# Optimization experiments

Hardware: AMD Instinct MI355X
Metric: run time of the kernel (lower is better)

## Reference

```python
import jax, jax.numpy as jnp
import numpy as np

S, D, H, E = 4096, 1024, 16, 64  # seq_len, embed_dim, n_heads, head_size


def setup_inputs() -> dict:
    key = jax.random.key(0)
    ks = jax.random.split(key, 8)
    s_d = 1.0 / np.sqrt(D).astype(np.float32)
    return {
        "x": jax.random.normal(ks[0], (S, D), jnp.float32),
        # per-head Q/K/V projections (no bias), stacked over heads: [H, D, E]
        "Wk": jax.random.normal(ks[1], (H, D, E), jnp.float32) * s_d,
        "Wq": jax.random.normal(ks[2], (H, D, E), jnp.float32) * s_d,
        "Wv": jax.random.normal(ks[3], (H, D, E), jnp.float32) * s_d,
        # output projection Dense(D) with bias
        "Wo": jax.random.normal(ks[4], (H * E, D), jnp.float32) * (1.0 / np.sqrt(H * E).astype(np.float32)),
        "bo": jnp.zeros((D,), jnp.float32),
        # MLP: Dense(4D) -> gelu -> Dense(D), both with bias
        "W1": jax.random.normal(ks[5], (D, 4 * D), jnp.float32) * s_d,
        "b1": jnp.zeros((4 * D,), jnp.float32),
        "W2": jax.random.normal(ks[6], (4 * D, D), jnp.float32) * (1.0 / np.sqrt(4 * D).astype(np.float32)),
        "b2": jnp.zeros((D,), jnp.float32),
    }


def _attention(x, Wk, Wq, Wv):
    # per-head projections, vectorized over heads (original loops in Python)
    k = jnp.einsum('sd,hde->hse', x, Wk)
    q = jnp.einsum('sd,hde->hse', x, Wq)
    v = jnp.einsum('sd,hde->hse', x, Wv)
    # NOTE: original computes keys @ queries.T -> scores[i, j] = k_i . q_j
    scores = jnp.einsum('hse,hte->hst', k, q) / jnp.sqrt(jnp.float32(E))
    mask = jnp.tril(jnp.ones((x.shape[0], x.shape[0]), dtype=bool))  # [S, S]
    w = jax.nn.softmax(jnp.where(mask, scores, -jnp.inf), axis=-1)   # [H, S, S]
    out = jnp.einsum('hst,hte->hse', w, v)                            # [H, S, E]
    # concatenate heads along feature axis (head 0 first, matching the loop)
    return out.transpose(1, 0, 2).reshape(x.shape[0], -1)             # [S, H*E]


def reference(x, Wk, Wq, Wv, Wo, bo, W1, b1, W2, b2):
    x = x + _attention(x, Wk, Wq, Wv) @ Wo + bo
    h = jax.nn.gelu(x @ W1 + b1, approximate=True)  # flax default gelu (tanh approx)
    return x + h @ W2 + b2
```

## Files before the change

### kernel.cpp

```cpp
#include <hip/hip_runtime.h>

typedef __attribute__((ext_vector_type(8))) short s16x8;
typedef __attribute__((ext_vector_type(4))) short s16x4;
typedef __attribute__((ext_vector_type(4))) float f32x4;


__device__ __forceinline__ unsigned short f2bf(float f) {
    union { float f; unsigned u; } v; v.f = f;
    unsigned r = v.u + 0x7FFFu + ((v.u >> 16) & 1u);
    return (unsigned short)(r >> 16);
}

__device__ __forceinline__ float bf2f(unsigned short b) {
    union { unsigned u; float f; } v; v.u = ((unsigned)b) << 16;
    return v.f;
}

__device__ __forceinline__ unsigned cvt_pk_bf16(float lo, float hi) {
    unsigned r;
    asm("v_cvt_pk_bf16_f32 %0, %1, %2" : "=v"(r) : "v"(lo), "v"(hi));
    return r;
}

__device__ __forceinline__ float exp2_fast(float x) {
    float r;
    asm("v_exp_f32 %0, %1" : "=v"(r) : "v"(x));
    return r;
}

__device__ __forceinline__ float gelu_tanh(float x) {
    float u = 0.7978845608028654f * (x + 0.044715f * x * x * x);
    float au = fabsf(u);
    float t = 1.f - 2.f / (__expf(2.f * au) + 1.f);
    t = (u < 0.f) ? -t : t;
    return 0.5f * x * (1.f + t);
}

__device__ __forceinline__ void load_lds16(const void* g, void* l) {
    __builtin_amdgcn_global_load_lds(
        (const __attribute__((address_space(1))) void*)g,
        (__attribute__((address_space(3))) void*)l, 16, 0, 0);
}

__device__ __forceinline__ void xcd_remap(int& bx, int& by) {
    const int gx = gridDim.x;
    const int nwg = gx * gridDim.y;
    const int id = by * gx + bx;
    const int nid = (id & 7) * (nwg >> 3) + (id >> 3);
    bx = nid % gx; by = nid / gx;
}


__global__ void convert_bf16_k(const float* __restrict__ in,
                               unsigned short* __restrict__ out, int n) {
    int i = (blockIdx.x * blockDim.x + threadIdx.x) * 4;
    if (i >= n) return;
    float4 v = *(const float4*)(in + i);
    ushort4 o;
    o.x = f2bf(v.x); o.y = f2bf(v.y); o.z = f2bf(v.z); o.w = f2bf(v.w);
    *(ushort4*)(out + i) = o;
}

__global__ void transpose_k(const float* __restrict__ in,
                            unsigned short* __restrict__ out, int R, int C) {
    __shared__ float tile[32][33];
    const int b = blockIdx.z;
    const int c0 = blockIdx.x * 32, r0 = blockIdx.y * 32;
    const float* inb = in + (size_t)b * R * C;
    unsigned short* outb = out + (size_t)b * R * C;
    const int tx = threadIdx.x, ty = threadIdx.y;
    #pragma unroll
    for (int i = 0; i < 4; ++i)
        tile[ty + i*8][tx] = inb[(size_t)(r0 + ty + i*8) * C + c0 + tx];
    __syncthreads();
    #pragma unroll
    for (int i = 0; i < 4; ++i)
        outb[(size_t)(c0 + ty + i*8) * R + r0 + tx] = f2bf(tile[tx][ty + i*8]);
}

template<int EPI>
__global__ __launch_bounds__(256) void gemm_bt(
    const unsigned short* __restrict__ A,
    const unsigned short* __restrict__ BT,
    const float* __restrict__ bias,
    const float* __restrict__ resid,
    float* __restrict__ Cf,
    unsigned short* __restrict__ Cb,
    int M, int N, int K, int klen)
{
    __shared__ unsigned short As[3][128 * 32];
    __shared__ unsigned short Bs[3][128 * 32];
    const int tid = threadIdx.x;
    const int w  = tid >> 6, l = tid & 63;
    const int wr = w >> 1,  wc = w & 1;
    const int lg = l >> 4,  ll = l & 15;
    int bx = blockIdx.x, by = blockIdx.y;
    xcd_remap(bx, by);
    const int m0 = by * 128, n0 = bx * 128;
    const int koff = (EPI == 5) ? (int)blockIdx.z * klen : 0;

    const int srow = w * 16 + (l >> 2);
    const int scol = (((l & 3) ^ ((l >> 2) & 3))) * 8;

    f32x4 acc[4][4] = {};

    auto stage = [&](int buf, int k0) {
        #pragma unroll
        for (int i = 0; i < 2; ++i) {
            load_lds16(A  + (size_t)(m0 + srow + i*64) * K + koff + k0 + scol,
                       (char*)As[buf] + i*4096 + w*1024);
            load_lds16(BT + (size_t)(n0 + srow + i*64) * K + koff + k0 + scol,
                       (char*)Bs[buf] + i*4096 + w*1024);
        }
    };

    const int nsteps = ((EPI == 5) ? klen : K) >> 5;
    stage(0, 0); stage(1, 32);
    int buf = 0;
    for (int s = 0; s < nsteps; ++s) {
        if (s + 1 < nsteps) asm volatile("s_waitcnt vmcnt(4)" ::: "memory");
        else                asm volatile("s_waitcnt vmcnt(0)" ::: "memory");
        __builtin_amdgcn_s_barrier();
        s16x8 a[4], b[4];
        #pragma unroll
        for (int m = 0; m < 4; ++m) {
            const int row = wr*64 + m*16 + ll;
            a[m] = *(const s16x8*)&As[buf][row * 32 + ((lg ^ (ll & 3)) * 8)];
        }
        #pragma unroll
        for (int n = 0; n < 4; ++n) {
            const int row = wc*64 + n*16 + ll;
            b[n] = *(const s16x8*)&Bs[buf][row * 32 + ((lg ^ (ll & 3)) * 8)];
        }
        int bnext = buf + 2; if (bnext >= 3) bnext -= 3;
        if (s + 2 < nsteps) stage(bnext, (s + 2) << 5);
        __builtin_amdgcn_s_setprio(1);
        #pragma unroll
        for (int m = 0; m < 4; ++m)
            #pragma unroll
            for (int n = 0; n < 4; ++n)
                acc[m][n] = __builtin_amdgcn_mfma_f32_16x16x32_bf16(a[m], b[n], acc[m][n], 0, 0, 0);
        __builtin_amdgcn_s_setprio(0);
        buf = (buf == 2) ? 0 : buf + 1;
    }

    unsigned short* Cbz = (EPI == 5) ? (Cb + (size_t)blockIdx.z * M * N) : Cb;
    #pragma unroll
    for (int m = 0; m < 4; ++m) {
        #pragma unroll
        for (int n = 0; n < 4; ++n) {
            const int col = n0 + wc*64 + n*16 + ll;
            #pragma unroll
            for (int r = 0; r < 4; ++r) {
                const int row = m0 + wr*64 + m*16 + lg*4 + r;
                float v = acc[m][n][r];
                if constexpr (EPI == 2) v = gelu_tanh(v + bias[col]);
                if constexpr (EPI == 4) v *= (col < 1024) ? 0.1803368801f : 1.0f;
                Cbz[(size_t)row * N + col] = f2bf(v);
            }
        }
    }
}

template<int EPI>
__global__ __launch_bounds__(256) void gemm_bt64(
    const unsigned short* __restrict__ A,
    const unsigned short* __restrict__ BT,
    const float* __restrict__ bias,
    const float* __restrict__ resid,
    float* __restrict__ Cf,
    unsigned short* __restrict__ Cb,
    int M, int N, int K)
{
    __shared__ unsigned short As[4][128 * 32];
    __shared__ unsigned short Bs[4][64 * 32];
    const int tid = threadIdx.x;
    const int w  = tid >> 6, l = tid & 63;
    const int lg = l >> 4,  ll = l & 15;
    int bx = blockIdx.x, by = blockIdx.y;
    xcd_remap(bx, by);
    const int m0 = by * 128, n0 = bx * 64;

    const int srowA = w * 16 + (l >> 2);
    const int scolA = (((l & 3) ^ ((l >> 2) & 3))) * 8;
    const int srowB = tid >> 2;
    const int scolB = (((tid & 3) ^ ((tid >> 2) & 3))) * 8;

    f32x4 acc[2][4] = {};

    auto stage = [&](int buf, int k0) {
        #pragma unroll
        for (int i = 0; i < 2; ++i)
            load_lds16(A + (size_t)(m0 + srowA + i*64) * K + k0 + scolA,
                       (char*)As[buf] + i*4096 + w*1024);
        load_lds16(BT + (size_t)(n0 + srowB) * K + k0 + scolB,
                   (char*)Bs[buf] + w*1024);
    };

    const int nsteps = K >> 5;
    stage(0, 0); stage(1, 32); stage(2, 64);
    int buf = 0;
    for (int s = 0; s < nsteps; ++s) {
        const int rem = nsteps - 1 - s;
        if (rem >= 2)      asm volatile("s_waitcnt vmcnt(6)" ::: "memory");
        else if (rem == 1) asm volatile("s_waitcnt vmcnt(3)" ::: "memory");
        else               asm volatile("s_waitcnt vmcnt(0)" ::: "memory");
        __builtin_amdgcn_s_barrier();
        s16x8 a[2], b[4];
        #pragma unroll
        for (int m = 0; m < 2; ++m) {
            const int row = w*32 + m*16 + ll;
            a[m] = *(const s16x8*)&As[buf][row * 32 + ((lg ^ (ll & 3)) * 8)];
        }
        #pragma unroll
        for (int n = 0; n < 4; ++n) {
            const int row = n*16 + ll;
            b[n] = *(const s16x8*)&Bs[buf][row * 32 + ((lg ^ (ll & 3)) * 8)];
        }
        int bnext = buf + 3; if (bnext >= 4) bnext -= 4;
        if (s + 3 < nsteps) stage(bnext, (s + 3) << 5);
        __builtin_amdgcn_s_setprio(1);
        #pragma unroll
        for (int m = 0; m < 2; ++m)
            #pragma unroll
            for (int n = 0; n < 4; ++n)
                acc[m][n] = __builtin_amdgcn_mfma_f32_16x16x32_bf16(a[m], b[n], acc[m][n], 0, 0, 0);
        __builtin_amdgcn_s_setprio(0);
        buf = (buf + 1) & 3;
    }

    #pragma unroll
    for (int m = 0; m < 2; ++m) {
        #pragma unroll
        for (int n = 0; n < 4; ++n) {
            const int col = n0 + n*16 + ll;
            #pragma unroll
            for (int r = 0; r < 4; ++r) {
                const int row = m0 + w*32 + m*16 + lg*4 + r;
                float v = acc[m][n][r];
                if constexpr (EPI == 1) v += bias[col] + resid[(size_t)row * N + col];
                Cb[(size_t)row * N + col] = f2bf(v);
                if constexpr (EPI == 1)
                    Cf[(size_t)row * N + col] = v;
            }
        }
    }
}

__global__ __launch_bounds__(256) void mlp2_combine_k(
    const unsigned short* __restrict__ P,
    const float* __restrict__ bias,
    const float* __restrict__ resid,
    float* __restrict__ out)
{
    const int idx = (blockIdx.x * 256 + threadIdx.x) * 4;
    const int col = idx & 1023;
    ushort4 a = *(const ushort4*)(P + idx);
    ushort4 b = *(const ushort4*)(P + 4194304 + idx);
    float4 rs = *(const float4*)(resid + idx);
    float4 o;
    o.x = bf2f(a.x) + bf2f(b.x) + bias[col]     + rs.x;
    o.y = bf2f(a.y) + bf2f(b.y) + bias[col + 1] + rs.y;
    o.z = bf2f(a.z) + bf2f(b.z) + bias[col + 2] + rs.z;
    o.w = bf2f(a.w) + bf2f(b.w) + bias[col + 3] + rs.w;
    *(float4*)(out + idx) = o;
}

__global__ __launch_bounds__(256) void attn_k(
    const unsigned short* __restrict__ Rq,
    const unsigned short* __restrict__ Ck,
    const unsigned short* __restrict__ Vt,
    unsigned short* __restrict__ Ppart,
    float* __restrict__ Lpart)
{
    __shared__ unsigned short Ks[3][64 * 64];
    __shared__ unsigned short Vs[3][64 * 64];

    const int bx = blockIdx.x;
    const int h  = bx & 15;
    const int j  = (bx >> 4) & 1;
    const int sb = 31 - (bx >> 5);
    const int t0 = j ? (sb + 1) : 0;
    const int t1 = j ? (2*sb + 2) : (sb + 1);

    const int tid = threadIdx.x;
    const int w = tid >> 6, l = tid & 63;
    const int lg = l >> 4, ll = l & 15;

    const int gsrc  = ((l & 7) ^ (l >> 3)) * 8;
    const int kOff0 = (w*16 +     (l >> 3)) * 2048 + h*64 + gsrc;
    const int kOff1 = (w*16 + 8 + (l >> 3)) * 2048 + h*64 + gsrc;
    const int vOff0 = (h*64 + w*16 +     (l >> 3)) * 4096 + gsrc;
    const int vOff1 = (h*64 + w*16 + 8 + (l >> 3)) * 4096 + gsrc;
    const int ldsOff = w * 2048;

    int qkoff[4][2];
    #pragma unroll
    for (int jj = 0; jj < 4; ++jj) {
        const int row = jj*16 + ll, r7 = row & 7;
        qkoff[jj][0] = row*128 + ((lg)     ^ r7) * 16;
        qkoff[jj][1] = row*128 + ((4 + lg) ^ r7) * 16;
    }
    int pvoff[4][2][2];
    #pragma unroll
    for (int n = 0; n < 4; ++n) {
        const int row = n*16 + ll, r7 = row & 7;
        #pragma unroll
        for (int c = 0; c < 2; ++c) {
            const int gl = (c*4     + (lg >> 1)) ^ r7;
            const int gh = (c*4 + 2 + (lg >> 1)) ^ r7;
            pvoff[n][c][0] = row*128 + gl*16 + (lg & 1)*8;
            pvoff[n][c][1] = row*128 + gh*16 + (lg & 1)*8;
        }
    }

    auto stage = [&](int t, int buf) {
        const unsigned short* qsrc = Ck + (size_t)t * 131072;
        const unsigned short* vsrc = Vt + t * 64;
        char* kd = (char*)Ks[buf] + ldsOff;
        char* vd = (char*)Vs[buf] + ldsOff;
        load_lds16(qsrc + kOff0, kd);
        load_lds16(qsrc + kOff1, kd + 1024);
        load_lds16(vsrc + vOff0, vd);
        load_lds16(vsrc + vOff1, vd + 1024);
    };

    const int row0 = sb*128 + w*32;
    const int qgA  = row0 + ll;
    const int qgB  = row0 + 16 + ll;
    const size_t rbA = (size_t)qgA * 2048 + h*64;
    const size_t rbB = (size_t)qgB * 2048 + h*64;
    const s16x8 rA0 = *(const s16x8*)&Rq[rbA + lg*8];
    const s16x8 rA1 = *(const s16x8*)&Rq[rbA + 32 + lg*8];
    const s16x8 rB0 = *(const s16x8*)&Rq[rbB + lg*8];
    const s16x8 rB1 = *(const s16x8*)&Rq[rbB + 32 + lg*8];

    const short onebf = (short)0x3F80;
    const s16x8 ones = {onebf, onebf, onebf, onebf, onebf, onebf, onebf, onebf};

    f32x4 o[2][4] = {};
    f32x4 o4[2] = {};

    stage(t0, 0);
    if (t0 + 1 < t1) stage(t0 + 1, 1);
    int buf = 0;

    for (int t = t0; t < t1; ++t) {
        if (t < t1-1) asm volatile("s_waitcnt vmcnt(4)" ::: "memory");
        else          asm volatile("s_waitcnt vmcnt(0)" ::: "memory");
        __builtin_amdgcn_s_barrier();
        const char* kb = (const char*)Ks[buf];
        const char* vb = (const char*)Vs[buf];
        const bool diag = (t >= 2*sb);

        f32x4 st[2][4];
        __builtin_amdgcn_s_setprio(1);
        #pragma unroll
        for (int jj = 0; jj < 4; ++jj) {
            s16x8 k0 = *(const s16x8*)(kb + qkoff[jj][0]);
            s16x8 k1 = *(const s16x8*)(kb + qkoff[jj][1]);
            f32x4 z = {0.f, 0.f, 0.f, 0.f};
            f32x4 ta = __builtin_amdgcn_mfma_f32_16x16x32_bf16(k0, rA0, z, 0, 0, 0);
            st[0][jj] = __builtin_amdgcn_mfma_f32_16x16x32_bf16(k1, rA1, ta, 0, 0, 0);
            f32x4 tb = __builtin_amdgcn_mfma_f32_16x16x32_bf16(k0, rB0, z, 0, 0, 0);
            st[1][jj] = __builtin_amdgcn_mfma_f32_16x16x32_bf16(k1, rB1, tb, 0, 0, 0);
        }
        __builtin_amdgcn_s_setprio(0);

        int bnext = buf + 2; if (bnext >= 3) bnext -= 3;
        if (t + 2 < t1) stage(t + 2, bnext);

        float p[2][4][4];
        if (diag) {
            #pragma unroll
            for (int jj = 0; jj < 4; ++jj)
                #pragma unroll
                for (int r = 0; r < 4; ++r) {
                    const int jg = t*64 + jj*16 + lg*4 + r;
                    p[0][jj][r] = exp2_fast((jg > qgA) ? -3e38f : st[0][jj][r]);
                    p[1][jj][r] = exp2_fast((jg > qgB) ? -3e38f : st[1][jj][r]);
                }
        } else {
            #pragma unroll
            for (int rs = 0; rs < 2; ++rs)
                #pragma unroll
                for (int jj = 0; jj < 4; ++jj)
                    #pragma unroll
                    for (int r = 0; r < 4; ++r)
                        p[rs][jj][r] = exp2_fast(st[rs][jj][r]);
        }

        s16x8 apv[2][2];
        #pragma unroll
        for (int rs = 0; rs < 2; ++rs)
            #pragma unroll
            for (int c = 0; c < 2; ++c) {
                union { unsigned u[4]; s16x8 v; } pk;
                pk.u[0] = cvt_pk_bf16(p[rs][2*c][0],   p[rs][2*c][1]);
                pk.u[1] = cvt_pk_bf16(p[rs][2*c][2],   p[rs][2*c][3]);
                pk.u[2] = cvt_pk_bf16(p[rs][2*c+1][0], p[rs][2*c+1][1]);
                pk.u[3] = cvt_pk_bf16(p[rs][2*c+1][2], p[rs][2*c+1][3]);
                apv[rs][c] = pk.v;
            }
        __builtin_amdgcn_s_setprio(1);
        #pragma unroll
        for (int rs = 0; rs < 2; ++rs) {
            o4[rs] = __builtin_amdgcn_mfma_f32_16x16x32_bf16(apv[rs][0], ones, o4[rs], 0, 0, 0);
            o4[rs] = __builtin_amdgcn_mfma_f32_16x16x32_bf16(apv[rs][1], ones, o4[rs], 0, 0, 0);
        }
        #pragma unroll
        for (int n = 0; n < 4; ++n) {
            #pragma unroll
            for (int c = 0; c < 2; ++c) {
                s16x4 lo = *(const s16x4*)(vb + pvoff[n][c][0]);
                s16x4 hi = *(const s16x4*)(vb + pvoff[n][c][1]);
                union { s16x4 h2[2]; s16x8 v; } u;
                u.h2[0] = lo; u.h2[1] = hi;
                o[0][n] = __builtin_amdgcn_mfma_f32_16x16x32_bf16(apv[0][c], u.v, o[0][n], 0, 0, 0);
                o[1][n] = __builtin_amdgcn_mfma_f32_16x16x32_bf16(apv[1][c], u.v, o[1][n], 0, 0, 0);
            }
        }
        __builtin_amdgcn_s_setprio(0);

        buf = (buf == 2) ? 0 : buf + 1;
    }

    unsigned short* Pout = Ppart + (size_t)j * 4194304;
    float* Lout = Lpart + (size_t)j * 65536;
    #pragma unroll
    for (int rs = 0; rs < 2; ++rs)
        #pragma unroll
        for (int r = 0; r < 4; ++r) {
            const int row = row0 + rs*16 + lg*4 + r;
            const size_t orow = (size_t)row * 1024 + h * 64;
            #pragma unroll
            for (int n = 0; n < 4; ++n)
                Pout[orow + n*16 + ll] = f2bf(o[rs][n][r]);
            if (ll == 0) Lout[row * 16 + h] = o4[rs][r];
        }
}

__global__ __launch_bounds__(256) void attn_combine_k(
    const unsigned short* __restrict__ P,
    const float* __restrict__ L,
    unsigned short* __restrict__ Out)
{
    const int idx = (blockIdx.x * 256 + threadIdx.x) * 4;
    const int row = idx >> 10, h = (idx & 1023) >> 6;
    const float inv = 1.f / (L[row*16 + h] + L[65536 + row*16 + h]);
    ushort4 a = *(const ushort4*)(P + idx);
    ushort4 b = *(const ushort4*)(P + 4194304 + idx);
    ushort4 o;
    o.x = f2bf((bf2f(a.x) + bf2f(b.x)) * inv);
    o.y = f2bf((bf2f(a.y) + bf2f(b.y)) * inv);
    o.z = f2bf((bf2f(a.z) + bf2f(b.z)) * inv);
    o.w = f2bf((bf2f(a.w) + bf2f(b.w)) * inv);
    *(ushort4*)(Out + idx) = o;
}


extern "C" void kernel_launch(void* const* d_in, const int* in_sizes, int n_in,
                              void* d_out, int out_size, void* d_ws, size_t ws_size,
                              hipStream_t stream) {
    const float* x  = (const float*)d_in[0];
    const float* Wk = (const float*)d_in[1];
    const float* Wq = (const float*)d_in[2];
    const float* Wv = (const float*)d_in[3];
    const float* Wo = (const float*)d_in[4];
    const float* bo = (const float*)d_in[5];
    const float* W1 = (const float*)d_in[6];
    const float* b1 = (const float*)d_in[7];
    const float* W2 = (const float*)d_in[8];
    const float* b2 = (const float*)d_in[9];
    float* out = (float*)d_out;

    char* ws = (char*)d_ws;
    unsigned short* x_bf  = (unsigned short*)(ws);
    unsigned short* WqkT  = (unsigned short*)(ws + (8u  << 20));
    unsigned short* WvT   = (unsigned short*)(ws + (12u << 20));
    unsigned short* WoT   = (unsigned short*)(ws + (14u << 20));
    unsigned short* W1T   = (unsigned short*)(ws + (16u << 20));
    unsigned short* W2T   = (unsigned short*)(ws + (24u << 20));
    unsigned short* QKm   = (unsigned short*)(ws + (32u << 20));
    unsigned short* attn  = (unsigned short*)(ws + (48u << 20));
    unsigned short* Vt    = (unsigned short*)(ws + (56u << 20));
    float*          yf    = (float*)(ws + (64u << 20));
    float*          Lpart = (float*)ws;
    unsigned short* Ppart = (unsigned short*)(ws + (64u << 20));
    unsigned short* Pmlp  = (unsigned short*)(ws);
    unsigned short* y_bf  = x_bf;
    unsigned short* h_bf  = QKm;

    dim3 tb(32, 8);
    convert_bf16_k<<<4096, 256, 0, stream>>>(x, x_bf, 4096 * 1024);
    transpose_k<<<dim3(2, 32, 16),  tb, 0, stream>>>(Wq, WqkT,               1024, 64);
    transpose_k<<<dim3(2, 32, 16),  tb, 0, stream>>>(Wk, WqkT + 1024 * 1024, 1024, 64);
    transpose_k<<<dim3(2, 32, 16),  tb, 0, stream>>>(Wv, WvT, 1024, 64);
    transpose_k<<<dim3(32, 32, 1),  tb, 0, stream>>>(Wo, WoT, 1024, 1024);
    transpose_k<<<dim3(128, 32, 1), tb, 0, stream>>>(W1, W1T, 1024, 4096);
    transpose_k<<<dim3(32, 128, 1), tb, 0, stream>>>(W2, W2T, 4096, 1024);

    gemm_bt<4><<<dim3(16, 32), 256, 0, stream>>>(x_bf, WqkT, nullptr, nullptr, nullptr,
                                                 QKm, 4096, 2048, 1024, 1024);
    gemm_bt64<0><<<dim3(64, 8), 256, 0, stream>>>(WvT, x_bf, nullptr, nullptr, nullptr,
                                                  Vt, 1024, 4096, 1024);

    attn_k<<<1024, 256, 0, stream>>>(QKm + 1024 , QKm , Vt, Ppart, Lpart);
    attn_combine_k<<<4096, 256, 0, stream>>>(Ppart, Lpart, attn);

    gemm_bt64<1><<<dim3(16, 32), 256, 0, stream>>>(attn, WoT, bo, x, yf, y_bf,
                                                   4096, 1024, 1024);
    gemm_bt<2><<<dim3(32, 32), 256, 0, stream>>>(y_bf, W1T, b1, nullptr, nullptr, h_bf,
                                                 4096, 4096, 1024, 1024);
    gemm_bt<5><<<dim3(8, 32, 2), 256, 0, stream>>>(h_bf, W2T, nullptr, nullptr, nullptr,
                                                   Pmlp, 4096, 1024, 4096, 2048);
    mlp2_combine_k<<<4096, 256, 0, stream>>>(Pmlp, b2, yf, out);
}
```

Before: 249.1 us.

## Double attention block to 256 query rows with 8 waves sharing K/V tiles

```diff
diff --git a/kernel.cpp b/kernel.cpp
--- a/kernel.cpp
+++ b/kernel.cpp
@@ -266,7 +266,7 @@
     *(float4*)(out + idx) = o;
 }
 
-__global__ __launch_bounds__(256) void attn_k(
+__global__ __launch_bounds__(512) void attn_k(
     const unsigned short* __restrict__ Rq,
     const unsigned short* __restrict__ Ck,
     const unsigned short* __restrict__ Vt,
@@ -279,20 +279,19 @@
     const int bx = blockIdx.x;
     const int h  = bx & 15;
     const int j  = (bx >> 4) & 1;
-    const int sb = 31 - (bx >> 5);
-    const int t0 = j ? (sb + 1) : 0;
-    const int t1 = j ? (2*sb + 2) : (sb + 1);
+    const int sb = 15 - (bx >> 5);
+    const int half = 2*sb + 2;
+    const int t0 = j ? half : 0;
+    const int t1 = j ? 2*half : half;
 
     const int tid = threadIdx.x;
     const int w = tid >> 6, l = tid & 63;
     const int lg = l >> 4, ll = l & 15;
 
     const int gsrc  = ((l & 7) ^ (l >> 3)) * 8;
-    const int kOff0 = (w*16 +     (l >> 3)) * 2048 + h*64 + gsrc;
-    const int kOff1 = (w*16 + 8 + (l >> 3)) * 2048 + h*64 + gsrc;
-    const int vOff0 = (h*64 + w*16 +     (l >> 3)) * 4096 + gsrc;
-    const int vOff1 = (h*64 + w*16 + 8 + (l >> 3)) * 4096 + gsrc;
-    const int ldsOff = w * 2048;
+    const int kOff  = (w*8 + (l >> 3)) * 2048 + h*64 + gsrc;
+    const int vOff  = (h*64 + w*8 + (l >> 3)) * 4096 + gsrc;
+    const int ldsOff = w * 1024;
 
     int qkoff[4][2];
     #pragma unroll
@@ -315,17 +314,11 @@
     }
 
     auto stage = [&](int t, int buf) {
-        const unsigned short* qsrc = Ck + (size_t)t * 131072;
-        const unsigned short* vsrc = Vt + t * 64;
-        char* kd = (char*)Ks[buf] + ldsOff;
-        char* vd = (char*)Vs[buf] + ldsOff;
-        load_lds16(qsrc + kOff0, kd);
-        load_lds16(qsrc + kOff1, kd + 1024);
-        load_lds16(vsrc + vOff0, vd);
-        load_lds16(vsrc + vOff1, vd + 1024);
+        load_lds16(Ck + (size_t)t * 131072 + kOff, (char*)Ks[buf] + ldsOff);
+        load_lds16(Vt + t * 64 + vOff,             (char*)Vs[buf] + ldsOff);
     };
 
-    const int row0 = sb*128 + w*32;
+    const int row0 = sb*256 + w*32;
     const int qgA  = row0 + ll;
     const int qgB  = row0 + 16 + ll;
     const size_t rbA = (size_t)qgA * 2048 + h*64;
@@ -342,85 +335,90 @@
     f32x4 o4[2] = {};
 
     stage(t0, 0);
-    if (t0 + 1 < t1) stage(t0 + 1, 1);
+    stage(t0 + 1, 1);
     int buf = 0;
 
     for (int t = t0; t < t1; ++t) {
-        if (t < t1-1) asm volatile("s_waitcnt vmcnt(4)" ::: "memory");
+        if (t < t1-1) asm volatile("s_waitcnt vmcnt(2)" ::: "memory");
         else          asm volatile("s_waitcnt vmcnt(0)" ::: "memory");
         __builtin_amdgcn_s_barrier();
         const char* kb = (const char*)Ks[buf];
         const char* vb = (const char*)Vs[buf];
-        const bool diag = (t >= 2*sb);
+        const bool live = (t*64 <= row0 + 31);
+        const bool anyMask = (t*64 + 63 > row0);
 
         f32x4 st[2][4];
-        __builtin_amdgcn_s_setprio(1);
-        #pragma unroll
-        for (int jj = 0; jj < 4; ++jj) {
-            s16x8 k0 = *(const s16x8*)(kb + qkoff[jj][0]);
-            s16x8 k1 = *(const s16x8*)(kb + qkoff[jj][1]);
-            f32x4 z = {0.f, 0.f, 0.f, 0.f};
-            f32x4 ta = __builtin_amdgcn_mfma_f32_16x16x32_bf16(k0, rA0, z, 0, 0, 0);
-            st[0][jj] = __builtin_amdgcn_mfma_f32_16x16x32_bf16(k1, rA1, ta, 0, 0, 0);
-            f32x4 tb = __builtin_amdgcn_mfma_f32_16x16x32_bf16(k0, rB0, z, 0, 0, 0);
-            st[1][jj] = __builtin_amdgcn_mfma_f32_16x16x32_bf16(k1, rB1, tb, 0, 0, 0);
-        }
-        __builtin_amdgcn_s_setprio(0);
+        if (live) {
+            __builtin_amdgcn_s_setprio(1);
+            #pragma unroll
+            for (int jj = 0; jj < 4; ++jj) {
+                s16x8 k0 = *(const s16x8*)(kb + qkoff[jj][0]);
+                s16x8 k1 = *(const s16x8*)(kb + qkoff[jj][1]);
+                f32x4 z = {0.f, 0.f, 0.f, 0.f};
+                f32x4 ta = __builtin_amdgcn_mfma_f32_16x16x32_bf16(k0, rA0, z, 0, 0, 0);
+                st[0][jj] = __builtin_amdgcn_mfma_f32_16x16x32_bf16(k1, rA1, ta, 0, 0, 0);
+                f32x4 tb = __builtin_amdgcn_mfma_f32_16x16x32_bf16(k0, rB0, z, 0, 0, 0);
+                st[1][jj] = __builtin_amdgcn_mfma_f32_16x16x32_bf16(k1, rB1, tb, 0, 0, 0);
+            }
+            __builtin_amdgcn_s_setprio(0);
+        }
 
         int bnext = buf + 2; if (bnext >= 3) bnext -= 3;
         if (t + 2 < t1) stage(t + 2, bnext);
 
-        float p[2][4][4];
-        if (diag) {
-            #pragma unroll
-            for (int jj = 0; jj < 4; ++jj)
-                #pragma unroll
-                for (int r = 0; r < 4; ++r) {
-                    const int jg = t*64 + jj*16 + lg*4 + r;
-                    p[0][jj][r] = exp2_fast((jg > qgA) ? -3e38f : st[0][jj][r]);
-                    p[1][jj][r] = exp2_fast((jg > qgB) ? -3e38f : st[1][jj][r]);
-                }
-        } else {
-            #pragma unroll
-            for (int rs = 0; rs < 2; ++rs)
+        if (live) {
+            float p[2][4][4];
+            if (anyMask) {
                 #pragma unroll
                 for (int jj = 0; jj < 4; ++jj)
                     #pragma unroll
-                    for (int r = 0; r < 4; ++r)
-                        p[rs][jj][r] = exp2_fast(st[rs][jj][r]);
-        }
-
-        s16x8 apv[2][2];
-        #pragma unroll
-        for (int rs = 0; rs < 2; ++rs)
-            #pragma unroll
-            for (int c = 0; c < 2; ++c) {
-                union { unsigned u[4]; s16x8 v; } pk;
-                pk.u[0] = cvt_pk_bf16(p[rs][2*c][0],   p[rs][2*c][1]);
-                pk.u[1] = cvt_pk_bf16(p[rs][2*c][2],   p[rs][2*c][3]);
-                pk.u[2] = cvt_pk_bf16(p[rs][2*c+1][0], p[rs][2*c+1][1]);
-                pk.u[3] = cvt_pk_bf16(p[rs][2*c+1][2], p[rs][2*c+1][3]);
-                apv[rs][c] = pk.v;
+                    for (int r = 0; r < 4; ++r) {
+                        const int jg = t*64 + jj*16 + lg*4 + r;
+                        p[0][jj][r] = exp2_fast((jg > qgA) ? -3e38f : st[0][jj][r]);
+                        p[1][jj][r] = exp2_fast((jg > qgB) ? -3e38f : st[1][jj][r]);
+                    }
+            } else {
+                #pragma unroll
+                for (int rs = 0; rs < 2; ++rs)
+                    #pragma unroll
+                    for (int jj = 0; jj < 4; ++jj)
+                        #pragma unroll
+                        for (int r = 0; r < 4; ++r)
+                            p[rs][jj][r] = exp2_fast(st[rs][jj][r]);
             }
-        __builtin_amdgcn_s_setprio(1);
-        #pragma unroll
-        for (int rs = 0; rs < 2; ++rs) {
-            o4[rs] = __builtin_amdgcn_mfma_f32_16x16x32_bf16(apv[rs][0], ones, o4[rs], 0, 0, 0);
-            o4[rs] = __builtin_amdgcn_mfma_f32_16x16x32_bf16(apv[rs][1], ones, o4[rs], 0, 0, 0);
-        }
-        #pragma unroll
-        for (int n = 0; n < 4; ++n) {
-            #pragma unroll
-            for (int c = 0; c < 2; ++c) {
-                s16x4 lo = *(const s16x4*)(vb + pvoff[n][c][0]);
-                s16x4 hi = *(const s16x4*)(vb + pvoff[n][c][1]);
-                union { s16x4 h2[2]; s16x8 v; } u;
-                u.h2[0] = lo; u.h2[1] = hi;
-                o[0][n] = __builtin_amdgcn_mfma_f32_16x16x32_bf16(apv[0][c], u.v, o[0][n], 0, 0, 0);
-                o[1][n] = __builtin_amdgcn_mfma_f32_16x16x32_bf16(apv[1][c], u.v, o[1][n], 0, 0, 0);
+
+            s16x8 apv[2][2];
+            #pragma unroll
+            for (int rs = 0; rs < 2; ++rs)
+                #pragma unroll
+                for (int c = 0; c < 2; ++c) {
+                    union { unsigned u[4]; s16x8 v; } pk;
+                    pk.u[0] = cvt_pk_bf16(p[rs][2*c][0],   p[rs][2*c][1]);
+                    pk.u[1] = cvt_pk_bf16(p[rs][2*c][2],   p[rs][2*c][3]);
+                    pk.u[2] = cvt_pk_bf16(p[rs][2*c+1][0], p[rs][2*c+1][1]);
+                    pk.u[3] = cvt_pk_bf16(p[rs][2*c+1][2], p[rs][2*c+1][3]);
+                    apv[rs][c] = pk.v;
+                }
+            __builtin_amdgcn_s_setprio(1);
+            #pragma unroll
+            for (int rs = 0; rs < 2; ++rs) {
+                o4[rs] = __builtin_amdgcn_mfma_f32_16x16x32_bf16(apv[rs][0], ones, o4[rs], 0, 0, 0);
+                o4[rs] = __builtin_amdgcn_mfma_f32_16x16x32_bf16(apv[rs][1], ones, o4[rs], 0, 0, 0);
             }
-        }
-        __builtin_amdgcn_s_setprio(0);
+            #pragma unroll
+            for (int n = 0; n < 4; ++n) {
+                #pragma unroll
+                for (int c = 0; c < 2; ++c) {
+                    s16x4 lo = *(const s16x4*)(vb + pvoff[n][c][0]);
+                    s16x4 hi = *(const s16x4*)(vb + pvoff[n][c][1]);
+                    union { s16x4 h2[2]; s16x8 v; } u;
+                    u.h2[0] = lo; u.h2[1] = hi;
+                    o[0][n] = __builtin_amdgcn_mfma_f32_16x16x32_bf16(apv[0][c], u.v, o[0][n], 0, 0, 0);
+                    o[1][n] = __builtin_amdgcn_mfma_f32_16x16x32_bf16(apv[1][c], u.v, o[1][n], 0, 0, 0);
+                }
+            }
+            __builtin_amdgcn_s_setprio(0);
+        }
 
         buf = (buf == 2) ? 0 : buf + 1;
     }
@@ -505,7 +503,7 @@
     gemm_bt64<0><<<dim3(64, 8), 256, 0, stream>>>(WvT, x_bf, nullptr, nullptr, nullptr,
                                                   Vt, 1024, 4096, 1024);
 
-    attn_k<<<1024, 256, 0, stream>>>(QKm + 1024 , QKm , Vt, Ppart, Lpart);
+    attn_k<<<512, 512, 0, stream>>>(QKm + 1024 , QKm , Vt, Ppart, Lpart);
     attn_combine_k<<<4096, 256, 0, stream>>>(Ppart, Lpart, attn);
 
     gemm_bt64<1><<<dim3(16, 32), 256, 0, stream>>>(attn, WoT, bo, x, yf, y_bf,
```

New measurement: 241.6 us. 3.0% less time.
